# Kernel tuning notes

Hardware: AMD Instinct MI355X
Metric: run time of the kernel (lower is better)

Reference implementation:

```python
import jax, jax.numpy as jnp
import numpy as np

N = 1_000_000
D_IN = 57   # hardcoded reshape(1,57) in original aggregate()
D_OUT = 128
K = 3       # num_sample=3 hardcoded in _get_unique_neighs_list


def _masked_mean_aggregate(h, neigh_idx, neigh_mask):
    # h: [N, D]; neigh_idx: [N, K] int; neigh_mask: [N, K] {0,1}
    feats = h[neigh_idx]                                   # [N, K, D] gather
    m = neigh_mask.astype(h.dtype)[..., None]              # [N, K, 1]
    s = jnp.sum(feats * m, axis=1)                         # [N, D]
    cnt = jnp.maximum(jnp.sum(neigh_mask, axis=1, keepdims=True).astype(h.dtype), 1.0)
    return s / cnt                                         # mask.mm(embed_matrix) equivalent (segment mean)


def _sage_layer(self_feats, aggregate_feats, W):
    # combined = cat([self, agg], dim=1); relu(W @ combined^T)^T; L2 normalize
    combined = jnp.concatenate([self_feats, aggregate_feats], axis=1)  # [N, 2D]
    out = jax.nn.relu(combined @ W.T)                                  # [N, out]
    norm = jnp.linalg.norm(out, axis=-1, keepdims=True)
    return out / jnp.maximum(norm, 1e-12)                              # F.normalize p=2 eps=1e-12


def setup_inputs() -> dict:
    key = jax.random.key(0)
    ks = jax.random.split(key, 7)
    x = jax.random.normal(ks[0], (N, D_IN), dtype=jnp.float32)
    W1 = jax.random.normal(ks[1], (D_OUT, 2 * D_IN), dtype=jnp.float32) * 0.1
    W2 = jax.random.normal(ks[2], (D_OUT, 2 * D_OUT), dtype=jnp.float32) * 0.1
    neigh_idx1 = jax.random.randint(ks[3], (N, K), 0, N, dtype=jnp.int32)
    neigh_mask1 = jax.random.randint(ks[4], (N, K), 0, 2, dtype=jnp.int32)
    neigh_idx2 = jax.random.randint(ks[5], (N, K), 0, N, dtype=jnp.int32)
    neigh_mask2 = jax.random.randint(ks[6], (N, K), 0, 2, dtype=jnp.int32)
    return {"x": x, "W1": W1, "W2": W2,
            "neigh_idx1": neigh_idx1, "neigh_mask1": neigh_mask1,
            "neigh_idx2": neigh_idx2, "neigh_mask2": neigh_mask2}


def reference(x, W1, W2, neigh_idx1, neigh_mask1, neigh_idx2, neigh_mask2):
    # Layer 1: aggregate over sampled neighbors of raw features, then SageLayer
    agg1 = _masked_mean_aggregate(x, neigh_idx1, neigh_mask1)
    h1 = _sage_layer(x, agg1, W1)                 # [N, D_OUT]
    # Layer 2
    agg2 = _masked_mean_aggregate(h1, neigh_idx2, neigh_mask2)
    h2 = _sage_layer(h1, agg2, W2)                # [N, D_OUT]
    return h2
```

## Files before the change

kernel.cpp:

```cpp
#include <hip/hip_runtime.h>
#include <hip/hip_bf16.h>

#define NN 1000000
#define NG 15625

typedef _Float16 f16x8 __attribute__((ext_vector_type(8)));
typedef _Float16 h2    __attribute__((ext_vector_type(2)));
typedef float f32x4    __attribute__((ext_vector_type(4)));
typedef unsigned short u16x8 __attribute__((ext_vector_type(8)));
typedef unsigned short u16x4 __attribute__((ext_vector_type(4)));

__device__ __forceinline__ unsigned short f2h(float v){
  _Float16 h = (_Float16)v; unsigned short s;
  __builtin_memcpy(&s, &h, 2); return s;
}

__global__ __launch_bounds__(512, 2) void sage2_mfma(
    const unsigned short* __restrict__ h1, const float* __restrict__ W2,
    const int* __restrict__ nidx, const int* __restrict__ nmask,
    float* __restrict__ out)
{
  __shared__ unsigned short comb[2][64 * 256];
  __shared__ float red[64][8];
  const int t   = threadIdx.x;
  const int l   = t & 63;
  const int w   = t >> 6;
  const int cfr = l & 15;
  const int kg  = l >> 4;

  f16x8 Bf[8];
  #pragma unroll
  for (int ks = 0; ks < 8; ++ks) {
    const int col = w*16 + cfr;
    const float* p = W2 + col*256 + ks*32 + kg*8;
    f32x4 a = *reinterpret_cast<const f32x4*>(p);
    f32x4 b = *reinterpret_cast<const f32x4*>(p + 4);
    f16x8 v;
    v[0]=(_Float16)a[0]; v[1]=(_Float16)a[1]; v[2]=(_Float16)a[2]; v[3]=(_Float16)a[3];
    v[4]=(_Float16)b[0]; v[5]=(_Float16)b[1]; v[6]=(_Float16)b[2]; v[7]=(_Float16)b[3];
    Bf[ks] = v;
  }

  const u16x8* hp = reinterpret_cast<const u16x8*>(h1);

  int nib0[2], nib1[2], nib2[2], nmb0[2], nmb1[2], nmb2[2];
  u16x8 sS[2], s0[2], s1[2], s2[2];
  _Float16 m0h[2], m1h[2], m2h[2], ivh[2];

  auto IDX = [&](int g){
    const long gb = (long)g * 64;
    #pragma unroll
    for (int i = 0; i < 2; ++i) {
      int n = (t + i*512) >> 4;
      long node = gb + n;
      nib0[i] = nidx[node*3+0]; nib1[i] = nidx[node*3+1]; nib2[i] = nidx[node*3+2];
      nmb0[i] = nmask[node*3+0]; nmb1[i] = nmask[node*3+1]; nmb2[i] = nmask[node*3+2];
    }
  };
  auto GATHER = [&](int g){
    const long gb = (long)g * 64;
    #pragma unroll
    for (int i = 0; i < 2; ++i) {
      int it = t + i*512;
      int n = it >> 4, q = it & 15;
      long node = gb + n;
      int b0 = nmb0[i], b1 = nmb1[i], b2 = nmb2[i];
      m0h[i]=(_Float16)(float)b0; m1h[i]=(_Float16)(float)b1; m2h[i]=(_Float16)(float)b2;
      int c = b0+b1+b2; ivh[i] = (_Float16)(1.0f/(float)(c<1?1:c));
      u16x8 z = {};
      sS[i] = hp[node*16 + q];
      s0[i] = b0 ? hp[(long)nib0[i]*16 + q] : z;
      s1[i] = b1 ? hp[(long)nib1[i]*16 + q] : z;
      s2[i] = b2 ? hp[(long)nib2[i]*16 + q] : z;
    }
  };
  auto UNPACK = [&](int p){
    char* cb = reinterpret_cast<char*>(comb[p]);
    #pragma unroll
    for (int i = 0; i < 2; ++i) {
      int it = t + i*512;
      int n = it >> 4, q = it & 15;
      int sw = (n & 7) << 4;
      *reinterpret_cast<u16x8*>(cb + n*512 + ((q*16) ^ sw)) = sS[i];
      h2 A[4], B4[4], C4[4], R[4];
      __builtin_memcpy(A,  &s0[i], 16);
      __builtin_memcpy(B4, &s1[i], 16);
      __builtin_memcpy(C4, &s2[i], 16);
      h2 M0 = {m0h[i], m0h[i]}, M1 = {m1h[i], m1h[i]},
         M2 = {m2h[i], m2h[i]}, IV = {ivh[i], ivh[i]};
      #pragma unroll
      for (int j = 0; j < 4; ++j)
        R[j] = (A[j]*M0 + B4[j]*M1 + C4[j]*M2) * IV;
      u16x8 r; __builtin_memcpy(&r, R, 16);
      *reinterpret_cast<u16x8*>(cb + n*512 + ((256 + q*16) ^ sw)) = r;
    }
  };

  const int g0 = blockIdx.x;
  IDX(g0); GATHER(g0);
  if (g0 + (int)gridDim.x < NG) IDX(g0 + gridDim.x);

  int p = 0;
  for (int g = g0; g < NG; g += gridDim.x) {
    const long gb = (long)g * 64;
    UNPACK(p);
    __syncthreads();

    int g1 = g + gridDim.x, g2 = g + 2*gridDim.x;
    if (g1 < NG) GATHER(g1);
    if (g2 < NG) IDX(g2);

    f32x4 acc[4];
    #pragma unroll
    for (int r = 0; r < 4; ++r) acc[r] = (f32x4){0.f,0.f,0.f,0.f};
    const int swz = (cfr & 7) << 4;
    char* cbp = reinterpret_cast<char*>(comb[p]);
    #pragma unroll
    for (int r = 0; r < 4; ++r) {
      const int rb = (r*16 + cfr) * 512;
      #pragma unroll
      for (int ks = 0; ks < 8; ++ks) {
        f16x8 af = *reinterpret_cast<const f16x8*>(cbp + rb + ((ks*64 + kg*16) ^ swz));
        acc[r] = __builtin_amdgcn_mfma_f32_16x16x32_f16(af, Bf[ks], acc[r], 0,0,0);
      }
    }

    float ssv[4][4];
    #pragma unroll
    for (int r = 0; r < 4; ++r) {
      #pragma unroll
      for (int e = 0; e < 4; ++e) {
        float v = fmaxf(acc[r][e], 0.f); acc[r][e] = v;
        float s = v*v;
        s += __shfl_xor(s, 1); s += __shfl_xor(s, 2);
        s += __shfl_xor(s, 4); s += __shfl_xor(s, 8);
        ssv[r][e] = s;
      }
      if (cfr < 4) {
        float v = cfr==0 ? ssv[r][0] : cfr==1 ? ssv[r][1] : cfr==2 ? ssv[r][2] : ssv[r][3];
        red[r*16 + kg*4 + cfr][w] = v;
      }
    }
    __syncthreads();

    #pragma unroll
    for (int r = 0; r < 4; ++r) {
      #pragma unroll
      for (int e = 0; e < 4; ++e) {
        int row = r*16 + kg*4 + e;
        f32x4 ra = *reinterpret_cast<const f32x4*>(&red[row][0]);
        f32x4 rb4 = *reinterpret_cast<const f32x4*>(&red[row][4]);
        float tot = (ra[0]+ra[1]) + (ra[2]+ra[3]) + (rb4[0]+rb4[1]) + (rb4[2]+rb4[3]);
        float inv = 1.0f / fmaxf(sqrtf(tot), 1e-12f);
        out[(gb + row)*128 + w*16 + cfr] = acc[r][e] * inv;
      }
    }
    p ^= 1;
  }
}

__global__ __launch_bounds__(256, 2) void sage1_mfma(
    const float* __restrict__ x, const float* __restrict__ W1,
    const int* __restrict__ nidx, const int* __restrict__ nmask,
    unsigned short* __restrict__ h1)
{
  __shared__ unsigned short comb[64 * 128];
  __shared__ float red[64][4];
  const int t   = threadIdx.x;
  const int l   = t & 63;
  const int w   = t >> 6;
  const int cfr = l & 15;
  const int kg  = l >> 4;

  f16x8 Bf[4][2];
  #pragma unroll
  for (int ks = 0; ks < 4; ++ks) {
    #pragma unroll
    for (int nf = 0; nf < 2; ++nf) {
      const int col = w*32 + nf*16 + cfr;
      const int k0  = ks*32 + kg*8;
      f16x8 v;
      #pragma unroll
      for (int j = 0; j < 8; ++j) {
        int lk = k0 + j;
        int wk = lk < 64 ? lk : lk - 7;
        bool valid = (lk < 57) || (lk >= 64 && lk < 121);
        v[j] = valid ? (_Float16)W1[col*114 + wk] : (_Float16)0.0f;
      }
      Bf[ks][nf] = v;
    }
  }

  char* cb = reinterpret_cast<char*>(comb);

  f32x4 sf[4], n0[4], n1[4], n2[4];
  float m0[4], m1[4], m2[4], iv[4];

  auto ISSUE = [&](int g){
    const long gb = (long)g * 64;
    #pragma unroll
    for (int i = 0; i < 4; ++i) {
      int it = t + i*256;
      int n = it >> 4, q = it & 15;
      long node = gb + n;
      int j0 = nidx[node*3+0], j1 = nidx[node*3+1], j2 = nidx[node*3+2];
      int b0 = nmask[node*3+0], b1 = nmask[node*3+1], b2 = nmask[node*3+2];
      m0[i]=(float)b0; m1[i]=(float)b1; m2[i]=(float)b2;
      int c = b0+b1+b2; iv[i] = 1.0f/(float)(c<1?1:c);
      #pragma unroll
      for (int jj = 0; jj < 4; ++jj) {
        int j = q*4 + jj;
        bool jv = j < 57;
        sf[i][jj] = jv         ? x[node*57 + j]     : 0.f;
        n0[i][jj] = (b0 && jv) ? x[(long)j0*57 + j] : 0.f;
        n1[i][jj] = (b1 && jv) ? x[(long)j1*57 + j] : 0.f;
        n2[i][jj] = (b2 && jv) ? x[(long)j2*57 + j] : 0.f;
      }
    }
  };

  if (blockIdx.x < NG) ISSUE(blockIdx.x);

  for (int g = blockIdx.x; g < NG; g += gridDim.x) {
    const long gb = (long)g * 64;
    #pragma unroll
    for (int i = 0; i < 4; ++i) {
      int it = t + i*256;
      int n = it >> 4, q = it & 15;
      int sw = (n & 7) << 4;
      u16x4 vs, va;
      #pragma unroll
      for (int jj = 0; jj < 4; ++jj) {
        vs[jj] = f2h(sf[i][jj]);
        va[jj] = f2h((m0[i]*n0[i][jj] + m1[i]*n1[i][jj] + m2[i]*n2[i][jj]) * iv[i]);
      }
      *reinterpret_cast<u16x4*>(cb + n*256 + ((q*8) ^ sw))       = vs;
      *reinterpret_cast<u16x4*>(cb + n*256 + ((128 + q*8) ^ sw)) = va;
    }
    __syncthreads();

    int gn = g + gridDim.x;
    if (gn < NG) ISSUE(gn);

    f32x4 acc[4][2];
    #pragma unroll
    for (int r = 0; r < 4; ++r) {
      acc[r][0] = (f32x4){0.f,0.f,0.f,0.f};
      acc[r][1] = (f32x4){0.f,0.f,0.f,0.f};
    }
    const int swz = (cfr & 7) << 4;
    #pragma unroll
    for (int r = 0; r < 4; ++r) {
      const int rb = (r*16 + cfr) * 256;
      #pragma unroll
      for (int ks = 0; ks < 4; ++ks) {
        f16x8 af = *reinterpret_cast<const f16x8*>(cb + rb + ((ks*64 + kg*16) ^ swz));
        acc[r][0] = __builtin_amdgcn_mfma_f32_16x16x32_f16(af, Bf[ks][0], acc[r][0], 0,0,0);
        acc[r][1] = __builtin_amdgcn_mfma_f32_16x16x32_f16(af, Bf[ks][1], acc[r][1], 0,0,0);
      }
    }

    float ssv[4][4];
    #pragma unroll
    for (int r = 0; r < 4; ++r) {
      #pragma unroll
      for (int e = 0; e < 4; ++e) {
        float v0 = fmaxf(acc[r][0][e], 0.f); acc[r][0][e] = v0;
        float v1 = fmaxf(acc[r][1][e], 0.f); acc[r][1][e] = v1;
        float s = v0*v0 + v1*v1;
        s += __shfl_xor(s, 1); s += __shfl_xor(s, 2);
        s += __shfl_xor(s, 4); s += __shfl_xor(s, 8);
        ssv[r][e] = s;
      }
      if (cfr < 4) {
        float v = cfr==0 ? ssv[r][0] : cfr==1 ? ssv[r][1] : cfr==2 ? ssv[r][2] : ssv[r][3];
        red[r*16 + kg*4 + cfr][w] = v;
      }
    }
    __syncthreads();

    #pragma unroll
    for (int r = 0; r < 4; ++r) {
      #pragma unroll
      for (int e = 0; e < 4; ++e) {
        int row = r*16 + kg*4 + e;
        float tot = red[row][0] + red[row][1] + red[row][2] + red[row][3];
        float inv = 1.0f / fmaxf(sqrtf(tot), 1e-12f);
        long node = gb + row;
        h1[node*128 + w*32 + cfr]      = f2h(acc[r][0][e] * inv);
        h1[node*128 + w*32 + 16 + cfr] = f2h(acc[r][1][e] * inv);
      }
    }
  }
}

extern "C" void kernel_launch(void* const* d_in, const int* in_sizes, int n_in,
                              void* d_out, int out_size, void* d_ws, size_t ws_size,
                              hipStream_t stream) {
  const float* x   = (const float*)d_in[0];
  const float* W1  = (const float*)d_in[1];
  const float* W2  = (const float*)d_in[2];
  const int* idx1  = (const int*)d_in[3];
  const int* msk1  = (const int*)d_in[4];
  const int* idx2  = (const int*)d_in[5];
  const int* msk2  = (const int*)d_in[6];
  float* out = (float*)d_out;
  unsigned short* h1 = (unsigned short*)d_ws;

  sage1_mfma<<<2048, 256, 0, stream>>>(x, W1, idx1, msk1, h1);
  sage2_mfma<<<512,  512, 0, stream>>>(h1, W2, idx2, msk2, out);
}
```

Baseline: 743.0 us.

## Stream layer-2 self features via direct global-to-LDS loads, restructure block to 256 threads

The layer-2 kernel now loads each node's own features straight into double-buffered LDS with global_load_lds instead of staging them through registers. Only the neighbour aggregation still goes through registers before being written to a separate LDS tile. Blocks shrink to 4 waves, each computing 32 output columns, and the grid grows to 768 with 3 blocks per SM. The separate index-prefetch stage is dropped, so index loads now sit in the gather's critical path. The intent is to cut register pressure and VGPR traffic and raise occupancy.

```diff
diff --git a/kernel.cpp b/kernel.cpp
--- a/kernel.cpp
+++ b/kernel.cpp
@@ -15,73 +15,79 @@
   __builtin_memcpy(&s, &h, 2); return s;
 }
 
-__global__ __launch_bounds__(512, 2) void sage2_mfma(
+__global__ __launch_bounds__(256, 3) void sage2_mfma(
     const unsigned short* __restrict__ h1, const float* __restrict__ W2,
     const int* __restrict__ nidx, const int* __restrict__ nmask,
     float* __restrict__ out)
 {
-  __shared__ unsigned short comb[2][64 * 256];
-  __shared__ float red[64][8];
+  __shared__ unsigned short selfS[2][64 * 128];
+  __shared__ unsigned short aggS[64 * 128];
+  __shared__ float red[64][4];
   const int t   = threadIdx.x;
   const int l   = t & 63;
   const int w   = t >> 6;
   const int cfr = l & 15;
   const int kg  = l >> 4;
 
-  f16x8 Bf[8];
+  f16x8 Bf[8][2];
   #pragma unroll
   for (int ks = 0; ks < 8; ++ks) {
-    const int col = w*16 + cfr;
-    const float* p = W2 + col*256 + ks*32 + kg*8;
-    f32x4 a = *reinterpret_cast<const f32x4*>(p);
-    f32x4 b = *reinterpret_cast<const f32x4*>(p + 4);
-    f16x8 v;
-    v[0]=(_Float16)a[0]; v[1]=(_Float16)a[1]; v[2]=(_Float16)a[2]; v[3]=(_Float16)a[3];
-    v[4]=(_Float16)b[0]; v[5]=(_Float16)b[1]; v[6]=(_Float16)b[2]; v[7]=(_Float16)b[3];
-    Bf[ks] = v;
+    #pragma unroll
+    for (int nf = 0; nf < 2; ++nf) {
+      const int col = w*32 + nf*16 + cfr;
+      const float* p = W2 + col*256 + ks*32 + kg*8;
+      f32x4 a = *reinterpret_cast<const f32x4*>(p);
+      f32x4 b = *reinterpret_cast<const f32x4*>(p + 4);
+      f16x8 v;
+      v[0]=(_Float16)a[0]; v[1]=(_Float16)a[1]; v[2]=(_Float16)a[2]; v[3]=(_Float16)a[3];
+      v[4]=(_Float16)b[0]; v[5]=(_Float16)b[1]; v[6]=(_Float16)b[2]; v[7]=(_Float16)b[3];
+      Bf[ks][nf] = v;
+    }
   }
 
   const u16x8* hp = reinterpret_cast<const u16x8*>(h1);
-
-  int nib0[2], nib1[2], nib2[2], nmb0[2], nmb1[2], nmb2[2];
-  u16x8 sS[2], s0[2], s1[2], s2[2];
-  _Float16 m0h[2], m1h[2], m2h[2], ivh[2];
-
-  auto IDX = [&](int g){
-    const long gb = (long)g * 64;
-    #pragma unroll
-    for (int i = 0; i < 2; ++i) {
-      int n = (t + i*512) >> 4;
-      long node = gb + n;
-      nib0[i] = nidx[node*3+0]; nib1[i] = nidx[node*3+1]; nib2[i] = nidx[node*3+2];
-      nmb0[i] = nmask[node*3+0]; nmb1[i] = nmask[node*3+1]; nmb2[i] = nmask[node*3+2];
-    }
-  };
+  char* aggB = reinterpret_cast<char*>(aggS);
+
+  u16x8 s0[4], s1[4], s2[4];
+  _Float16 m0h[4], m1h[4], m2h[4], ivh[4];
+
   auto GATHER = [&](int g){
     const long gb = (long)g * 64;
     #pragma unroll
-    for (int i = 0; i < 2; ++i) {
-      int it = t + i*512;
+    for (int i = 0; i < 4; ++i) {
+      int it = t + i*256;
       int n = it >> 4, q = it & 15;
       long node = gb + n;
-      int b0 = nmb0[i], b1 = nmb1[i], b2 = nmb2[i];
+      int j0 = nidx[node*3+0], j1 = nidx[node*3+1], j2 = nidx[node*3+2];
+      int b0 = nmask[node*3+0], b1 = nmask[node*3+1], b2 = nmask[node*3+2];
       m0h[i]=(_Float16)(float)b0; m1h[i]=(_Float16)(float)b1; m2h[i]=(_Float16)(float)b2;
       int c = b0+b1+b2; ivh[i] = (_Float16)(1.0f/(float)(c<1?1:c));
       u16x8 z = {};
-      sS[i] = hp[node*16 + q];
-      s0[i] = b0 ? hp[(long)nib0[i]*16 + q] : z;
-      s1[i] = b1 ? hp[(long)nib1[i]*16 + q] : z;
-      s2[i] = b2 ? hp[(long)nib2[i]*16 + q] : z;
+      s0[i] = b0 ? hp[(long)j0*16 + q] : z;
+      s1[i] = b1 ? hp[(long)j1*16 + q] : z;
+      s2[i] = b2 ? hp[(long)j2*16 + q] : z;
     }
   };
-  auto UNPACK = [&](int p){
-    char* cb = reinterpret_cast<char*>(comb[p]);
-    #pragma unroll
-    for (int i = 0; i < 2; ++i) {
-      int it = t + i*512;
+  auto SELF_DMA = [&](int g, int pp){
+    #pragma unroll
+    for (int i = 0; i < 4; ++i) {
+      int it = t + i*256;
+      int nn = it >> 4, qq0 = it & 15;
+      long node = (long)g * 64 + nn;
+      int qq = qq0 ^ (nn & 7);
+      const unsigned short* gp = h1 + node*128 + qq*8;
+      unsigned short* lp = &selfS[pp][it*8];
+      __builtin_amdgcn_global_load_lds(
+          (const __attribute__((address_space(1))) unsigned short*)gp,
+          (__attribute__((address_space(3))) unsigned short*)lp, 16, 0, 0);
+    }
+  };
+  auto UNPACK_AGG = [&](){
+    #pragma unroll
+    for (int i = 0; i < 4; ++i) {
+      int it = t + i*256;
       int n = it >> 4, q = it & 15;
       int sw = (n & 7) << 4;
-      *reinterpret_cast<u16x8*>(cb + n*512 + ((q*16) ^ sw)) = sS[i];
       h2 A[4], B4[4], C4[4], R[4];
       __builtin_memcpy(A,  &s0[i], 16);
       __builtin_memcpy(B4, &s1[i], 16);
@@ -92,36 +98,44 @@
       for (int j = 0; j < 4; ++j)
         R[j] = (A[j]*M0 + B4[j]*M1 + C4[j]*M2) * IV;
       u16x8 r; __builtin_memcpy(&r, R, 16);
-      *reinterpret_cast<u16x8*>(cb + n*512 + ((256 + q*16) ^ sw)) = r;
+      *reinterpret_cast<u16x8*>(aggB + n*256 + ((q*16) ^ sw)) = r;
     }
   };
 
   const int g0 = blockIdx.x;
-  IDX(g0); GATHER(g0);
-  if (g0 + (int)gridDim.x < NG) IDX(g0 + gridDim.x);
+  GATHER(g0); SELF_DMA(g0, 0);
 
   int p = 0;
   for (int g = g0; g < NG; g += gridDim.x) {
     const long gb = (long)g * 64;
-    UNPACK(p);
+    UNPACK_AGG();
     __syncthreads();
 
-    int g1 = g + gridDim.x, g2 = g + 2*gridDim.x;
-    if (g1 < NG) GATHER(g1);
-    if (g2 < NG) IDX(g2);
-
-    f32x4 acc[4];
-    #pragma unroll
-    for (int r = 0; r < 4; ++r) acc[r] = (f32x4){0.f,0.f,0.f,0.f};
+    int g1 = g + gridDim.x;
+    if (g1 < NG) { SELF_DMA(g1, p ^ 1); GATHER(g1); }
+
+    f32x4 acc[4][2];
+    #pragma unroll
+    for (int r = 0; r < 4; ++r) {
+      acc[r][0] = (f32x4){0.f,0.f,0.f,0.f};
+      acc[r][1] = (f32x4){0.f,0.f,0.f,0.f};
+    }
     const int swz = (cfr & 7) << 4;
-    char* cbp = reinterpret_cast<char*>(comb[p]);
-    #pragma unroll
-    for (int r = 0; r < 4; ++r) {
-      const int rb = (r*16 + cfr) * 512;
-      #pragma unroll
-      for (int ks = 0; ks < 8; ++ks) {
-        f16x8 af = *reinterpret_cast<const f16x8*>(cbp + rb + ((ks*64 + kg*16) ^ swz));
-        acc[r] = __builtin_amdgcn_mfma_f32_16x16x32_f16(af, Bf[ks], acc[r], 0,0,0);
+    char* selfB = reinterpret_cast<char*>(selfS) + p*(64*256);
+    #pragma unroll
+    for (int r = 0; r < 4; ++r) {
+      const int rb = (r*16 + cfr) * 256;
+      #pragma unroll
+      for (int ks = 0; ks < 4; ++ks) {
+        f16x8 af = *reinterpret_cast<const f16x8*>(selfB + rb + ((ks*64 + kg*16) ^ swz));
+        acc[r][0] = __builtin_amdgcn_mfma_f32_16x16x32_f16(af, Bf[ks][0], acc[r][0], 0,0,0);
+        acc[r][1] = __builtin_amdgcn_mfma_f32_16x16x32_f16(af, Bf[ks][1], acc[r][1], 0,0,0);
+      }
+      #pragma unroll
+      for (int ks = 0; ks < 4; ++ks) {
+        f16x8 af = *reinterpret_cast<const f16x8*>(aggB + rb + ((ks*64 + kg*16) ^ swz));
+        acc[r][0] = __builtin_amdgcn_mfma_f32_16x16x32_f16(af, Bf[ks+4][0], acc[r][0], 0,0,0);
+        acc[r][1] = __builtin_amdgcn_mfma_f32_16x16x32_f16(af, Bf[ks+4][1], acc[r][1], 0,0,0);
       }
     }
 
@@ -130,8 +144,9 @@
     for (int r = 0; r < 4; ++r) {
       #pragma unroll
       for (int e = 0; e < 4; ++e) {
-        float v = fmaxf(acc[r][e], 0.f); acc[r][e] = v;
-        float s = v*v;
+        float v0 = fmaxf(acc[r][0][e], 0.f); acc[r][0][e] = v0;
+        float v1 = fmaxf(acc[r][1][e], 0.f); acc[r][1][e] = v1;
+        float s = v0*v0 + v1*v1;
         s += __shfl_xor(s, 1); s += __shfl_xor(s, 2);
         s += __shfl_xor(s, 4); s += __shfl_xor(s, 8);
         ssv[r][e] = s;
@@ -148,11 +163,10 @@
       #pragma unroll
       for (int e = 0; e < 4; ++e) {
         int row = r*16 + kg*4 + e;
-        f32x4 ra = *reinterpret_cast<const f32x4*>(&red[row][0]);
-        f32x4 rb4 = *reinterpret_cast<const f32x4*>(&red[row][4]);
-        float tot = (ra[0]+ra[1]) + (ra[2]+ra[3]) + (rb4[0]+rb4[1]) + (rb4[2]+rb4[3]);
+        float tot = red[row][0] + red[row][1] + red[row][2] + red[row][3];
         float inv = 1.0f / fmaxf(sqrtf(tot), 1e-12f);
-        out[(gb + row)*128 + w*16 + cfr] = acc[r][e] * inv;
+        out[(gb + row)*128 + w*32 + cfr]      = acc[r][0][e] * inv;
+        out[(gb + row)*128 + w*32 + 16 + cfr] = acc[r][1][e] * inv;
       }
     }
     p ^= 1;
@@ -308,5 +322,5 @@
   unsigned short* h1 = (unsigned short*)d_ws;
 
   sage1_mfma<<<2048, 256, 0, stream>>>(x, W1, idx1, msk1, h1);
-  sage2_mfma<<<512,  512, 0, stream>>>(h1, W2, idx2, msk2, out);
+  sage2_mfma<<<768,  256, 0, stream>>>(h1, W2, idx2, msk2, out);
 }
```

Result: slower. 1.099 ms (+48.0%).
